# Kernel tuning notes

Measured on AMD Instinct MI355X. Metric: run time of the kernel, lower is better.

The kernel has to match this reference:

```python
import jax, jax.numpy as jnp
import numpy as np

IN_DIMS = (8, 8, 8, 8)
OUT_DIMS = (8, 8, 8, 8)
RANK = 8
IN_FEATURES = 4096
OUT_FEATURES = 4096
BATCH = 4096


def setup_inputs() -> dict:
    key = jax.random.key(0)
    ks = jax.random.split(key, 6)
    scale = 1.0 / (IN_FEATURES ** 0.5)
    d = len(IN_DIMS)
    ranks = (1,) + (RANK,) * (d - 1) + (1,)
    cores = {}
    for k in range(d):
        shape = (ranks[k], IN_DIMS[k], OUT_DIMS[k], ranks[k + 1])
        # roughly balanced per-core scale so the dense-equivalent weight has ~1/sqrt(N) scale
        c_scale = scale ** (1.0 / d)
        cores[f"core_{k}"] = (jax.random.normal(ks[k + 1], shape, dtype=jnp.float32) * c_scale)
    x = jax.random.normal(ks[0], (BATCH, IN_FEATURES), dtype=jnp.float32)
    bias = jnp.zeros((OUT_FEATURES,), dtype=jnp.float32)
    return {"x": x, **cores, "bias": bias}


def _tt_contract(x, cores):
    # x: (B, N) with N = prod(IN_DIMS). Cores: core_k (r_{k-1}, i_k, o_k, r_k).
    # y[b, o1..od] = sum_{i,r} prod_k core_k[r_{k-1}, i_k, o_k, r_k] * x[b, i1..id]
    B = x.shape[0]
    d = len(IN_DIMS)
    # z: (Bo, r, i_k, suffix) where Bo = B * prod(out dims already contracted)
    z = x.reshape(B, 1, IN_DIMS[0], -1)
    for k, core in enumerate(cores):
        # contract current input mode and left rank against the core
        z = jnp.einsum("bris,riok->boks", z, core)  # (Bo, o_k, r_k, suffix)
        if k + 1 < d:
            Bo, ok, rk, s = z.shape
            z = z.reshape(Bo * ok, rk, IN_DIMS[k + 1], s // IN_DIMS[k + 1])
    return z.reshape(B, -1)  # (B, prod(OUT_DIMS))


def reference(x, core_0, core_1, core_2, core_3, bias):
    in_dtype = x.dtype
    xc = x.astype(core_0.dtype)
    y = _tt_contract(xc, (core_0, core_1, core_2, core_3))
    y = y + bias
    return y.astype(in_dtype)
```

## Files before the change

### kernel.cpp

```cpp
#include <hip/hip_runtime.h>
#include <hip/hip_bf16.h>


typedef __attribute__((ext_vector_type(8))) short bf16x8;
typedef __attribute__((ext_vector_type(16))) float f32x16;

#define MFMA32(a, b, c) __builtin_amdgcn_mfma_f32_32x32x16_bf16(a, b, c, 0, 0, 0)

__device__ __forceinline__ unsigned short bfu(float f) {
    __hip_bfloat16 h = __float2bfloat16(f);
    return *reinterpret_cast<unsigned short*>(&h);
}
__device__ __forceinline__ unsigned pk2(float a, float b) {
    return (unsigned)bfu(a) | ((unsigned)bfu(b) << 16);
}

__global__ void tt_prep(const float* __restrict__ c0, const float* __restrict__ c1,
                        const float* __restrict__ c2, const float* __restrict__ c3,
                        unsigned short* __restrict__ wpack) {
    int e    = blockIdx.x * 256 + threadIdx.x;
    int lane = (e >> 3) & 63;
    int j    = e & 7;
    int hi   = lane >> 5, l31 = lane & 31;
    float acc = 0.f;
    if (e < 32768) {
        int idx = e;
        int r2  = idx >> 12;
        int nt  = (idx >> 11) & 1;
        int ks1 = (idx >> 9) & 3;
        int i23 = ks1 * 16 + hi * 8 + j;
        int o23 = nt * 32 + l31;
        int i2 = i23 >> 3, i3 = i23 & 7, o2 = o23 >> 3, o3 = o23 & 7;
        #pragma unroll
        for (int r3 = 0; r3 < 8; ++r3)
            acc += c2[((r2 * 8 + i2) * 8 + o2) * 8 + r3] * c3[(r3 * 8 + i3) * 8 + o3];
    } else {
        int idx = e - 32768;
        int r2  = idx >> 12;
        int mt2 = (idx >> 11) & 1;
        int kt  = (idx >> 10) & 1;
        int ks2 = (idx >> 9) & 1;
        int i01 = kt * 32 + ks2 * 16 + hi * 8 + j;
        int o01 = mt2 * 32 + l31;
        int i0 = i01 >> 3, i1 = i01 & 7, o0 = o01 >> 3, o1 = o01 & 7;
        #pragma unroll
        for (int r1 = 0; r1 < 8; ++r1)
            acc += c0[(i0 * 8 + o0) * 8 + r1] * c1[((r1 * 8 + i1) * 8 + o1) * 8 + r2];
    }
    wpack[e] = bfu(acc);
}

__global__ __launch_bounds__(256, 2)
void tt_main(const float* __restrict__ x, const float* __restrict__ bias,
             const unsigned short* __restrict__ wpack, float* __restrict__ out) {
    const int lane = threadIdx.x & 63;
    const int wave = threadIdx.x >> 6;
    const int b    = blockIdx.x * 4 + wave;
    const int l31  = lane & 31;
    const int hi   = lane >> 5;

    const float* xb = x + (size_t)b * 4096;

    bf16x8 xa[2][4];
    #pragma unroll
    for (int mt = 0; mt < 2; ++mt)
        #pragma unroll
        for (int ks1 = 0; ks1 < 4; ++ks1) {
            const float* p = xb + (mt * 32 + l31) * 64 + ks1 * 16 + hi * 8;
            float4 u0 = *(const float4*)p;
            float4 u1 = *(const float4*)(p + 4);
            union { unsigned w[4]; bf16x8 v; } t;
            t.w[0] = pk2(u0.x, u0.y);
            t.w[1] = pk2(u0.z, u0.w);
            t.w[2] = pk2(u1.x, u1.y);
            t.w[3] = pk2(u1.z, u1.w);
            xa[mt][ks1] = t.v;
        }

    f32x16 yacc[2][2];
    #pragma unroll
    for (int i = 0; i < 2; ++i)
        #pragma unroll
        for (int k = 0; k < 2; ++k)
            yacc[i][k] = (f32x16)0.0f;

    const bf16x8* Vp = (const bf16x8*)wpack;
    const bf16x8* Up = (const bf16x8*)(wpack + 32768);

    for (int r2 = 0; r2 < 8; ++r2) {
        bf16x8 vf[2][4];
        #pragma unroll
        for (int nt = 0; nt < 2; ++nt)
            #pragma unroll
            for (int ks1 = 0; ks1 < 4; ++ks1)
                vf[nt][ks1] = Vp[((r2 * 2 + nt) * 4 + ks1) * 64 + lane];

        #pragma unroll
        for (int mt = 0; mt < 2; ++mt) {
            bf16x8 uf[2][2];
            #pragma unroll
            for (int mt2 = 0; mt2 < 2; ++mt2)
                #pragma unroll
                for (int ks2 = 0; ks2 < 2; ++ks2)
                    uf[mt2][ks2] = Up[(((r2 * 2 + mt2) * 2 + mt) * 2 + ks2) * 64 + lane];

            #pragma unroll
            for (int nt = 0; nt < 2; ++nt) {
                f32x16 s = (f32x16)0.0f;
                #pragma unroll
                for (int ks1 = 0; ks1 < 4; ++ks1)
                    s = MFMA32(xa[mt][ks1], vf[nt][ks1], s);

                bf16x8 bf[2];
                #pragma unroll
                for (int ks2 = 0; ks2 < 2; ++ks2) {
                    unsigned A0 = pk2(s[8 * ks2 + 0], s[8 * ks2 + 1]);
                    unsigned B0 = pk2(s[8 * ks2 + 2], s[8 * ks2 + 3]);
                    unsigned A1 = pk2(s[8 * ks2 + 4], s[8 * ks2 + 5]);
                    unsigned B1 = pk2(s[8 * ks2 + 6], s[8 * ks2 + 7]);
                    auto rA = __builtin_amdgcn_permlane32_swap((int)A0, (int)A1, false, false);
                    auto rB = __builtin_amdgcn_permlane32_swap((int)B0, (int)B1, false, false);
                    union { unsigned w[4]; bf16x8 v; } t;
                    t.w[0] = (unsigned)rA[0];
                    t.w[1] = (unsigned)rB[0];
                    t.w[2] = (unsigned)rA[1];
                    t.w[3] = (unsigned)rB[1];
                    bf[ks2] = t.v;
                }

                #pragma unroll
                for (int mt2 = 0; mt2 < 2; ++mt2)
                    #pragma unroll
                    for (int ks2 = 0; ks2 < 2; ++ks2)
                        yacc[mt2][nt] = MFMA32(uf[mt2][ks2], bf[ks2], yacc[mt2][nt]);
            }
        }
    }

    float* ob = out + (size_t)b * 4096;
    #pragma unroll
    for (int mt2 = 0; mt2 < 2; ++mt2)
        #pragma unroll
        for (int nt = 0; nt < 2; ++nt)
            #pragma unroll
            for (int r = 0; r < 16; ++r) {
                int o01 = mt2 * 32 + (r & 3) + 8 * (r >> 2) + 4 * hi;
                int o23 = nt * 32 + l31;
                int off = o01 * 64 + o23;
                ob[off] = yacc[mt2][nt][r] + bias[off];
            }
}

extern "C" void kernel_launch(void* const* d_in, const int* in_sizes, int n_in,
                              void* d_out, int out_size, void* d_ws, size_t ws_size,
                              hipStream_t stream) {
    const float* x    = (const float*)d_in[0];
    const float* c0   = (const float*)d_in[1];
    const float* c1   = (const float*)d_in[2];
    const float* c2   = (const float*)d_in[3];
    const float* c3   = (const float*)d_in[4];
    const float* bias = (const float*)d_in[5];
    unsigned short* wpack = (unsigned short*)d_ws;

    tt_prep<<<256, 256, 0, stream>>>(c0, c1, c2, c3, wpack);
    tt_main<<<1024, 256, 0, stream>>>(x, bias, wpack, (float*)d_out);
}
```

Baseline: 145.7 us.

## Stage packed TT weights into LDS with double-buffered async global loads

Each block now copies the per-rank packed V and U weight fragments into a double-buffered shared-memory area with async global-to-LDS loads, prefetching the next rank while computing the current one. MFMA operands then come from LDS instead of every wave issuing its own global loads for the same weights. Launch bounds are raised to three blocks per SM for occupancy. The cost is a block-wide barrier each iteration and 32KB of LDS per block, which may limit occupancy.

```diff
diff --git a/kernel.cpp b/kernel.cpp
--- a/kernel.cpp
+++ b/kernel.cpp
@@ -13,6 +13,13 @@
 }
 __device__ __forceinline__ unsigned pk2(float a, float b) {
     return (unsigned)bfu(a) | ((unsigned)bfu(b) << 16);
+}
+
+__device__ __forceinline__ void gload_lds16(const char* g, char* l) {
+    __builtin_amdgcn_global_load_lds(
+        (const __attribute__((address_space(1))) unsigned int*)g,
+        (__attribute__((address_space(3))) unsigned int*)l,
+        16, 0, 0);
 }
 
 __global__ void tt_prep(const float* __restrict__ c0, const float* __restrict__ c1,
@@ -50,17 +57,31 @@
     wpack[e] = bfu(acc);
 }
 
-__global__ __launch_bounds__(256, 2)
+__device__ __forceinline__ void stage_r2(const char* wp, char* sm, int r2,
+                                         int wave, int lane) {
+    int isU = wave >> 1;
+    int f0  = (wave & 1) * 4;
+    const char* src = wp + isU * 65536 + (r2 * 8 + f0) * 1024 + lane * 16;
+    char* dst = sm + isU * 8192 + f0 * 1024;
+    #pragma unroll
+    for (int i = 0; i < 4; ++i)
+        gload_lds16(src + i * 1024, dst + i * 1024);
+}
+
+__global__ __launch_bounds__(256, 3)
 void tt_main(const float* __restrict__ x, const float* __restrict__ bias,
              const unsigned short* __restrict__ wpack, float* __restrict__ out) {
+    __shared__ __attribute__((aligned(16))) char smem[2][16384];
     const int lane = threadIdx.x & 63;
     const int wave = threadIdx.x >> 6;
     const int b    = blockIdx.x * 4 + wave;
     const int l31  = lane & 31;
     const int hi   = lane >> 5;
+    const char* wp = (const char*)wpack;
+
+    stage_r2(wp, smem[0], 0, wave, lane);
 
     const float* xb = x + (size_t)b * 4096;
-
     bf16x8 xa[2][4];
     #pragma unroll
     for (int mt = 0; mt < 2; ++mt)
@@ -84,16 +105,17 @@
         for (int k = 0; k < 2; ++k)
             yacc[i][k] = (f32x16)0.0f;
 
-    const bf16x8* Vp = (const bf16x8*)wpack;
-    const bf16x8* Up = (const bf16x8*)(wpack + 32768);
+    __syncthreads();
 
+    #pragma unroll
     for (int r2 = 0; r2 < 8; ++r2) {
-        bf16x8 vf[2][4];
-        #pragma unroll
-        for (int nt = 0; nt < 2; ++nt)
-            #pragma unroll
-            for (int ks1 = 0; ks1 < 4; ++ks1)
-                vf[nt][ks1] = Vp[((r2 * 2 + nt) * 4 + ks1) * 64 + lane];
+        const char* cur = smem[r2 & 1];
+        char*       nxt = smem[(r2 & 1) ^ 1];
+        if (r2 < 7)
+            stage_r2(wp, nxt, r2 + 1, wave, lane);
+
+        const char* vb = cur + lane * 16;
+        const char* ub = cur + 8192 + lane * 16;
 
         #pragma unroll
         for (int mt = 0; mt < 2; ++mt) {
@@ -102,14 +124,15 @@
             for (int mt2 = 0; mt2 < 2; ++mt2)
                 #pragma unroll
                 for (int ks2 = 0; ks2 < 2; ++ks2)
-                    uf[mt2][ks2] = Up[(((r2 * 2 + mt2) * 2 + mt) * 2 + ks2) * 64 + lane];
+                    uf[mt2][ks2] = *(const bf16x8*)(ub + (((mt2 * 2 + mt) * 2 + ks2) << 10));
 
             #pragma unroll
             for (int nt = 0; nt < 2; ++nt) {
                 f32x16 s = (f32x16)0.0f;
                 #pragma unroll
                 for (int ks1 = 0; ks1 < 4; ++ks1)
-                    s = MFMA32(xa[mt][ks1], vf[nt][ks1], s);
+                    s = MFMA32(xa[mt][ks1],
+                               *(const bf16x8*)(vb + ((nt * 4 + ks1) << 10)), s);
 
                 bf16x8 bf[2];
                 #pragma unroll
@@ -135,6 +158,7 @@
                         yacc[mt2][nt] = MFMA32(uf[mt2][ks2], bf[ks2], yacc[mt2][nt]);
             }
         }
+        __syncthreads();
     }
 
     float* ob = out + (size_t)b * 4096;
```

Result: slower. 162.9 us (+11.8%).
